# Performance work log

Measured on AMD Instinct MI355X. Metric: run time of the kernel, lower is better.

Reference implementation:

```python
import jax, jax.numpy as jnp
import numpy as np

N_NODES = 50000
N_EDGES = 800000
D = 128


def setup_inputs() -> dict:
    key = jax.random.key(0)
    k1, k2, k3, k4, k5 = jax.random.split(key, 5)
    feature = jax.random.normal(k1, (N_NODES, D), dtype=jnp.float32)
    src = jax.random.randint(k2, (N_EDGES,), 0, N_NODES, dtype=jnp.int64)
    dst = jax.random.randint(k3, (N_EDGES,), 0, N_NODES, dtype=jnp.int64)
    # Linear(in_feats=128, out_feats=128) params
    W = jax.random.normal(k4, (D, D), dtype=jnp.float32) * (1.0 / np.sqrt(D))
    b = jax.random.normal(k5, (D,), dtype=jnp.float32) * 0.01
    return {"feature": feature, "src": src, "dst": dst, "W": W, "b": b}


def reference(feature, src, dst, W, b):
    n = feature.shape[0]
    # copy_src message: each edge carries h[src]; segment-mean over in-edges at dst
    msgs = feature[src]                                      # [E, D] irregular gather
    summed = jax.ops.segment_sum(msgs, dst, num_segments=n)  # [N, D] scatter-add
    cnt = jax.ops.segment_sum(jnp.ones((src.shape[0],), dtype=feature.dtype),
                              dst, num_segments=n)           # in-degree per node
    h = summed / jnp.clip(cnt, 1.0)[:, None]                 # mean (isolated nodes -> 0)
    # NodeApplyModule: ReLU(W h + b)
    return jax.nn.relu(h @ W.T + b)
```

## Files before the change

### kernel.cpp

```cpp
#include <hip/hip_runtime.h>

#define NN 50000
#define NE 800000
#define DD 128
#define NPAD 50176


__global__ __launch_bounds__(256) void k_hist(const int* __restrict__ dst,
                                              int* __restrict__ cnt) {
  int e = blockIdx.x * 256 + threadIdx.x;
  if (e < NE) atomicAdd(&cnt[dst[e]], 1);
}

__global__ __launch_bounds__(256) void k_reduce(const int* __restrict__ cnt,
                                                int* __restrict__ bsum) {
  __shared__ int sh[256];
  int t = threadIdx.x;
  sh[t] = cnt[blockIdx.x * 256 + t];
  __syncthreads();
  for (int o = 128; o > 0; o >>= 1) {
    if (t < o) sh[t] += sh[t + o];
    __syncthreads();
  }
  if (t == 0) bsum[blockIdx.x] = sh[0];
}

__global__ __launch_bounds__(256) void k_scan_bsum(const int* __restrict__ bsum,
                                                   int* __restrict__ bsumx) {
  __shared__ int sh[256];
  int t = threadIdx.x;
  int v = (t < 196) ? bsum[t] : 0;
  sh[t] = v;
  __syncthreads();
  for (int o = 1; o < 256; o <<= 1) {
    int x = (t >= o) ? sh[t - o] : 0;
    __syncthreads();
    sh[t] += x;
    __syncthreads();
  }
  bsumx[t] = sh[t] - v;
}

__global__ __launch_bounds__(256) void k_scan_block(const int* __restrict__ cnt,
                                                    const int* __restrict__ bsumx,
                                                    int* __restrict__ pos) {
  __shared__ int sh[256];
  int t = threadIdx.x;
  int g = blockIdx.x * 256 + t;
  int v = cnt[g];
  sh[t] = v;
  __syncthreads();
  for (int o = 1; o < 256; o <<= 1) {
    int x = (t >= o) ? sh[t - o] : 0;
    __syncthreads();
    sh[t] += x;
    __syncthreads();
  }
  pos[g] = bsumx[blockIdx.x] + sh[t] - v;
}

__global__ __launch_bounds__(256) void k_fill(const int* __restrict__ src,
                                              const int* __restrict__ dst,
                                              int* __restrict__ pos,
                                              int* __restrict__ csr) {
  int e = blockIdx.x * 256 + threadIdx.x;
  if (e < NE) {
    int d = dst[e];
    int p = atomicAdd(&pos[d], 1);
    csr[p] = src[e];
  }
}

__global__ __launch_bounds__(256) void k_gather(const float* __restrict__ feat,
                                                const int* __restrict__ csr,
                                                const int* __restrict__ pos,
                                                const int* __restrict__ cnt,
                                                float* __restrict__ sum) {
  int n = blockIdx.x * 4 + (threadIdx.x >> 6);
  int lane = threadIdx.x & 63;
  int end = pos[n];
  int c = cnt[n];
  float ax = 0.f, ay = 0.f;
  for (int base = end - c; base < end; base += 64) {
    int m = end - base;
    if (m > 64) m = 64;
    int s = (base + lane < end) ? csr[base + lane] : 0;
    int j = 0;
    for (; j + 3 < m; j += 4) {
      int s0 = __shfl(s, j), s1 = __shfl(s, j + 1);
      int s2 = __shfl(s, j + 2), s3 = __shfl(s, j + 3);
      float2 v0 = ((const float2*)(feat + (long long)s0 * DD))[lane];
      float2 v1 = ((const float2*)(feat + (long long)s1 * DD))[lane];
      float2 v2 = ((const float2*)(feat + (long long)s2 * DD))[lane];
      float2 v3 = ((const float2*)(feat + (long long)s3 * DD))[lane];
      ax += (v0.x + v1.x) + (v2.x + v3.x);
      ay += (v0.y + v1.y) + (v2.y + v3.y);
    }
    for (; j < m; ++j) {
      int sj = __shfl(s, j);
      float2 v = ((const float2*)(feat + (long long)sj * DD))[lane];
      ax += v.x;
      ay += v.y;
    }
  }
  float2 o;
  o.x = ax;
  o.y = ay;
  ((float2*)(sum + (long long)n * DD))[lane] = o;
}

__global__ __launch_bounds__(256) void k_scatter(const float* __restrict__ feat,
                                                 const int* __restrict__ src,
                                                 const int* __restrict__ dst,
                                                 float* __restrict__ summed,
                                                 int* __restrict__ cnt) {
  int wave = threadIdx.x >> 6;
  int lane = threadIdx.x & 63;
  int e = blockIdx.x * 4 + wave;
  if (e >= NE) return;
  int s = src[e];
  int d = dst[e];
  float2 v = ((const float2*)(feat + (long long)s * DD))[lane];
  float* op = summed + (long long)d * DD + lane * 2;
  atomicAdd(op, v.x);
  atomicAdd(op + 1, v.y);
  if (lane == 0) atomicAdd(&cnt[d], 1);
}

__global__ __launch_bounds__(256) void k_gemm(float* __restrict__ io,
                                              const int* __restrict__ cnt,
                                              const float* __restrict__ W,
                                              const float* __restrict__ bias) {
  __shared__ float Wt[64][132];
  __shared__ __attribute__((aligned(16))) float hs[64][72];
  int tid = threadIdx.x;
  int row0 = blockIdx.x * 64;
  int tc = tid & 31;
  int tr = tid >> 5;

  float acc[8][4] = {};

  for (int p = 0; p < 2; ++p) {
    if (p) __syncthreads();
    for (int i = 0; i < 8; ++i) {
      int fidx = tid + (i << 8);
      int c = fidx >> 4;
      int kq = fidx & 15;
      float4 w = ((const float4*)W)[c * 32 + p * 16 + kq];
      int kk = kq << 2;
      Wt[kk + 0][c ^ (((kk + 0) & 31) << 2)] = w.x;
      Wt[kk + 1][c ^ (((kk + 1) & 31) << 2)] = w.y;
      Wt[kk + 2][c ^ (((kk + 2) & 31) << 2)] = w.z;
      Wt[kk + 3][c ^ (((kk + 3) & 31) << 2)] = w.w;
    }
    for (int i = 0; i < 4; ++i) {
      int fidx = tid + (i << 8);
      int r = fidx & 63;
      int kq = fidx >> 6;
      int grow = row0 + r;
      float4 v = make_float4(0.f, 0.f, 0.f, 0.f);
      if (grow < NN) {
        v = ((const float4*)io)[(long long)grow * 32 + p * 16 + kq];
        float inv = 1.0f / fmaxf((float)cnt[grow], 1.0f);
        v.x *= inv; v.y *= inv; v.z *= inv; v.w *= inv;
      }
      int kk = kq << 2;
      hs[kk + 0][r] = v.x;
      hs[kk + 1][r] = v.y;
      hs[kk + 2][r] = v.z;
      hs[kk + 3][r] = v.w;
    }
    __syncthreads();

#pragma unroll 4
    for (int kk = 0; kk < 64; ++kk) {
      float4 w4 = *(const float4*)&Wt[kk][(tc << 2) ^ ((kk & 31) << 2)];
      float4 h0 = *(const float4*)&hs[kk][tr << 3];
      float4 h1 = *(const float4*)&hs[kk][(tr << 3) + 4];
      acc[0][0] += h0.x * w4.x; acc[0][1] += h0.x * w4.y; acc[0][2] += h0.x * w4.z; acc[0][3] += h0.x * w4.w;
      acc[1][0] += h0.y * w4.x; acc[1][1] += h0.y * w4.y; acc[1][2] += h0.y * w4.z; acc[1][3] += h0.y * w4.w;
      acc[2][0] += h0.z * w4.x; acc[2][1] += h0.z * w4.y; acc[2][2] += h0.z * w4.z; acc[2][3] += h0.z * w4.w;
      acc[3][0] += h0.w * w4.x; acc[3][1] += h0.w * w4.y; acc[3][2] += h0.w * w4.z; acc[3][3] += h0.w * w4.w;
      acc[4][0] += h1.x * w4.x; acc[4][1] += h1.x * w4.y; acc[4][2] += h1.x * w4.z; acc[4][3] += h1.x * w4.w;
      acc[5][0] += h1.y * w4.x; acc[5][1] += h1.y * w4.y; acc[5][2] += h1.y * w4.z; acc[5][3] += h1.y * w4.w;
      acc[6][0] += h1.z * w4.x; acc[6][1] += h1.z * w4.y; acc[6][2] += h1.z * w4.z; acc[6][3] += h1.z * w4.w;
      acc[7][0] += h1.w * w4.x; acc[7][1] += h1.w * w4.y; acc[7][2] += h1.w * w4.z; acc[7][3] += h1.w * w4.w;
    }
  }

  float4 b4 = ((const float4*)bias)[tc];
#pragma unroll
  for (int r = 0; r < 8; ++r) {
    int row = row0 + (tr << 3) + r;
    if (row < NN) {
      float4 o;
      o.x = fmaxf(acc[r][0] + b4.x, 0.f);
      o.y = fmaxf(acc[r][1] + b4.y, 0.f);
      o.z = fmaxf(acc[r][2] + b4.z, 0.f);
      o.w = fmaxf(acc[r][3] + b4.w, 0.f);
      ((float4*)(io + (long long)row * DD))[tc] = o;
    }
  }
}

extern "C" void kernel_launch(void* const* d_in, const int* in_sizes, int n_in,
                              void* d_out, int out_size, void* d_ws, size_t ws_size,
                              hipStream_t stream) {
  const float* feature = (const float*)d_in[0];
  const int*   src     = (const int*)d_in[1];
  const int*   dst     = (const int*)d_in[2];
  const float* W       = (const float*)d_in[3];
  const float* bias    = (const float*)d_in[4];
  float* out = (float*)d_out;
  int* cnt = (int*)d_ws;

  size_t need = (size_t)(2 * NPAD + 512 + NE) * sizeof(int);
  int nblk_e = (NE + 255) / 256;
  int nblk_gemm = (NN + 63) / 64;

  if (ws_size >= need) {
    int* pos   = cnt + NPAD;
    int* bsum  = pos + NPAD;
    int* bsumx = bsum + 256;
    int* csr   = bsumx + 256;
    hipMemsetAsync(cnt, 0, NPAD * sizeof(int), stream);
    hipLaunchKernelGGL(k_hist, dim3(nblk_e), dim3(256), 0, stream, dst, cnt);
    hipLaunchKernelGGL(k_reduce, dim3(196), dim3(256), 0, stream, cnt, bsum);
    hipLaunchKernelGGL(k_scan_bsum, dim3(1), dim3(256), 0, stream, bsum, bsumx);
    hipLaunchKernelGGL(k_scan_block, dim3(196), dim3(256), 0, stream, cnt, bsumx, pos);
    hipLaunchKernelGGL(k_fill, dim3(nblk_e), dim3(256), 0, stream, src, dst, pos, csr);
    hipLaunchKernelGGL(k_gather, dim3(NN / 4), dim3(256), 0, stream,
                       feature, csr, pos, cnt, out);
    hipLaunchKernelGGL(k_gemm, dim3(nblk_gemm), dim3(256), 0, stream,
                       out, cnt, W, bias);
  } else {
    hipMemsetAsync(out, 0, (size_t)NN * DD * sizeof(float), stream);
    hipMemsetAsync(cnt, 0, NN * sizeof(int), stream);
    hipLaunchKernelGGL(k_scatter, dim3((NE + 3) / 4), dim3(256), 0, stream,
                       feature, src, dst, out, cnt);
    hipLaunchKernelGGL(k_gemm, dim3(nblk_gemm), dim3(256), 0, stream,
                       out, cnt, W, bias);
  }
}
```

Measured before the change: 261.7 us.

## Apply linear transform before aggregation and fuse mean, bias, ReLU into gather

The matmul moves ahead of the aggregation (W·mean(h) = mean(W·h)). A new register-tiled GEMM first computes feature·Wᵀ into a workspace buffer, and the CSR gather then averages those rows while applying bias and ReLU in the same kernel. The three-kernel prefix scan is replaced by a single 1024-thread block scan, and the gather uses float4 loads with two half-waves covering alternate edges. This removes the separate in-place GEMM pass over the aggregated output and two launches, but adds an extra 25.6MB workspace buffer write and needs more workspace.

```diff
diff --git a/kernel.cpp b/kernel.cpp
--- a/kernel.cpp
+++ b/kernel.cpp
@@ -12,51 +12,27 @@
   if (e < NE) atomicAdd(&cnt[dst[e]], 1);
 }
 
-__global__ __launch_bounds__(256) void k_reduce(const int* __restrict__ cnt,
-                                                int* __restrict__ bsum) {
-  __shared__ int sh[256];
+__global__ __launch_bounds__(1024) void k_scan1(const int* __restrict__ cnt,
+                                                int* __restrict__ pos) {
+  __shared__ int sh[1024];
   int t = threadIdx.x;
-  sh[t] = cnt[blockIdx.x * 256 + t];
+  int base = t * 49;
+  int ssum = 0;
+  for (int i = 0; i < 49; ++i) ssum += cnt[base + i];
+  sh[t] = ssum;
   __syncthreads();
-  for (int o = 128; o > 0; o >>= 1) {
-    if (t < o) sh[t] += sh[t + o];
-    __syncthreads();
-  }
-  if (t == 0) bsum[blockIdx.x] = sh[0];
-}
-
-__global__ __launch_bounds__(256) void k_scan_bsum(const int* __restrict__ bsum,
-                                                   int* __restrict__ bsumx) {
-  __shared__ int sh[256];
-  int t = threadIdx.x;
-  int v = (t < 196) ? bsum[t] : 0;
-  sh[t] = v;
-  __syncthreads();
-  for (int o = 1; o < 256; o <<= 1) {
+  for (int o = 1; o < 1024; o <<= 1) {
     int x = (t >= o) ? sh[t - o] : 0;
     __syncthreads();
     sh[t] += x;
     __syncthreads();
   }
-  bsumx[t] = sh[t] - v;
-}
-
-__global__ __launch_bounds__(256) void k_scan_block(const int* __restrict__ cnt,
-                                                    const int* __restrict__ bsumx,
-                                                    int* __restrict__ pos) {
-  __shared__ int sh[256];
-  int t = threadIdx.x;
-  int g = blockIdx.x * 256 + t;
-  int v = cnt[g];
-  sh[t] = v;
-  __syncthreads();
-  for (int o = 1; o < 256; o <<= 1) {
-    int x = (t >= o) ? sh[t - o] : 0;
-    __syncthreads();
-    sh[t] += x;
-    __syncthreads();
-  }
-  pos[g] = bsumx[blockIdx.x] + sh[t] - v;
+  int run = sh[t] - ssum;
+  for (int i = 0; i < 49; ++i) {
+    int v = cnt[base + i];
+    pos[base + i] = run;
+    run += v;
+  }
 }
 
 __global__ __launch_bounds__(256) void k_fill(const int* __restrict__ src,
@@ -71,11 +47,132 @@
   }
 }
 
-__global__ __launch_bounds__(256) void k_gather(const float* __restrict__ feat,
-                                                const int* __restrict__ csr,
-                                                const int* __restrict__ pos,
-                                                const int* __restrict__ cnt,
-                                                float* __restrict__ sum) {
+#define FMA8(R, H)                                          \
+  {                                                         \
+    acc[R][0] += (H)*w0.x; acc[R][1] += (H)*w0.y;           \
+    acc[R][2] += (H)*w0.z; acc[R][3] += (H)*w0.w;           \
+    acc[R][4] += (H)*w1.x; acc[R][5] += (H)*w1.y;           \
+    acc[R][6] += (H)*w1.z; acc[R][7] += (H)*w1.w;           \
+  }
+
+__global__ __launch_bounds__(256) void k_gemmT(const float* __restrict__ feat,
+                                               const float* __restrict__ W,
+                                               float* __restrict__ g) {
+  __shared__ float fs[32][260];
+  __shared__ float ws[32][132];
+  int tid = threadIdx.x;
+  int row0 = blockIdx.x * 256;
+  int tc = tid & 15;
+  int tr = tid >> 4;
+  float acc[16][8] = {};
+
+  for (int kc = 0; kc < 4; ++kc) {
+    if (kc) __syncthreads();
+    for (int i = 0; i < 8; ++i) {
+      int fidx = tid + (i << 8);
+      int r = fidx >> 3;
+      int q = fidx & 7;
+      int grow = row0 + r;
+      float4 v = make_float4(0.f, 0.f, 0.f, 0.f);
+      if (grow < NN) v = ((const float4*)feat)[grow * 32 + kc * 8 + q];
+      int k = q << 2;
+      fs[k + 0][r] = v.x;
+      fs[k + 1][r] = v.y;
+      fs[k + 2][r] = v.z;
+      fs[k + 3][r] = v.w;
+    }
+    for (int i = 0; i < 4; ++i) {
+      int fidx = tid + (i << 8);
+      int c = fidx >> 3;
+      int q = fidx & 7;
+      float4 v = ((const float4*)W)[c * 32 + kc * 8 + q];
+      int k = q << 2;
+      ws[k + 0][c] = v.x;
+      ws[k + 1][c] = v.y;
+      ws[k + 2][c] = v.z;
+      ws[k + 3][c] = v.w;
+    }
+    __syncthreads();
+
+#pragma unroll 8
+    for (int k = 0; k < 32; ++k) {
+      float4 w0 = *(const float4*)&ws[k][tc * 8];
+      float4 w1 = *(const float4*)&ws[k][tc * 8 + 4];
+      float4 h0 = *(const float4*)&fs[k][tr * 16];
+      float4 h1 = *(const float4*)&fs[k][tr * 16 + 4];
+      float4 h2 = *(const float4*)&fs[k][tr * 16 + 8];
+      float4 h3 = *(const float4*)&fs[k][tr * 16 + 12];
+      FMA8(0, h0.x) FMA8(1, h0.y) FMA8(2, h0.z) FMA8(3, h0.w)
+      FMA8(4, h1.x) FMA8(5, h1.y) FMA8(6, h1.z) FMA8(7, h1.w)
+      FMA8(8, h2.x) FMA8(9, h2.y) FMA8(10, h2.z) FMA8(11, h2.w)
+      FMA8(12, h3.x) FMA8(13, h3.y) FMA8(14, h3.z) FMA8(15, h3.w)
+    }
+  }
+
+#pragma unroll
+  for (int r = 0; r < 16; ++r) {
+    int grow = row0 + tr * 16 + r;
+    if (grow < NN) {
+      float4 o0, o1;
+      o0.x = acc[r][0]; o0.y = acc[r][1]; o0.z = acc[r][2]; o0.w = acc[r][3];
+      o1.x = acc[r][4]; o1.y = acc[r][5]; o1.z = acc[r][6]; o1.w = acc[r][7];
+      float4* gp = (float4*)(g + (long long)grow * DD) + tc * 2;
+      gp[0] = o0;
+      gp[1] = o1;
+    }
+  }
+}
+
+__global__ __launch_bounds__(256) void k_gmean(const float* __restrict__ g,
+                                               const int* __restrict__ csr,
+                                               const int* __restrict__ pos,
+                                               const int* __restrict__ cnt,
+                                               const float* __restrict__ bias,
+                                               float* __restrict__ out) {
+  int n = blockIdx.x * 4 + (threadIdx.x >> 6);
+  int lane = threadIdx.x & 63;
+  int half = lane >> 5;
+  int l32 = lane & 31;
+  int end = pos[n];
+  int c = cnt[n];
+  float4 a = make_float4(0.f, 0.f, 0.f, 0.f);
+  for (int base = end - c; base < end; base += 64) {
+    int m = end - base;
+    if (m > 64) m = 64;
+    int s = (base + lane < end) ? csr[base + lane] : 0;
+    for (int j = 0; j < m; j += 8) {
+#pragma unroll
+      for (int u = 0; u < 4; ++u) {
+        int j2 = j + 2 * u + half;
+        int sj = __shfl(s, j2);
+        if (j2 < m) {
+          float4 v = ((const float4*)(g + (long long)sj * DD))[l32];
+          a.x += v.x; a.y += v.y; a.z += v.z; a.w += v.w;
+        }
+      }
+    }
+  }
+  a.x += __shfl_xor(a.x, 32);
+  a.y += __shfl_xor(a.y, 32);
+  a.z += __shfl_xor(a.z, 32);
+  a.w += __shfl_xor(a.w, 32);
+  if (half == 0) {
+    float inv = 1.0f / fmaxf((float)c, 1.0f);
+    float4 b4 = ((const float4*)bias)[l32];
+    float4 o;
+    o.x = fmaxf(a.x * inv + b4.x, 0.f);
+    o.y = fmaxf(a.y * inv + b4.y, 0.f);
+    o.z = fmaxf(a.z * inv + b4.z, 0.f);
+    o.w = fmaxf(a.w * inv + b4.w, 0.f);
+    ((float4*)(out + (long long)n * DD))[l32] = o;
+  }
+}
+
+__global__ __launch_bounds__(256) void k_gather_sum(const float* __restrict__ feat,
+                                                    const int* __restrict__ csr,
+                                                    const int* __restrict__ pos,
+                                                    const int* __restrict__ cnt,
+                                                    float* __restrict__ sum) {
   int n = blockIdx.x * 4 + (threadIdx.x >> 6);
   int lane = threadIdx.x & 63;
   int end = pos[n];
@@ -109,37 +206,17 @@
   ((float2*)(sum + (long long)n * DD))[lane] = o;
 }
 
-__global__ __launch_bounds__(256) void k_scatter(const float* __restrict__ feat,
-                                                 const int* __restrict__ src,
-                                                 const int* __restrict__ dst,
-                                                 float* __restrict__ summed,
-                                                 int* __restrict__ cnt) {
-  int wave = threadIdx.x >> 6;
-  int lane = threadIdx.x & 63;
-  int e = blockIdx.x * 4 + wave;
-  if (e >= NE) return;
-  int s = src[e];
-  int d = dst[e];
-  float2 v = ((const float2*)(feat + (long long)s * DD))[lane];
-  float* op = summed + (long long)d * DD + lane * 2;
-  atomicAdd(op, v.x);
-  atomicAdd(op + 1, v.y);
-  if (lane == 0) atomicAdd(&cnt[d], 1);
-}
-
-__global__ __launch_bounds__(256) void k_gemm(float* __restrict__ io,
-                                              const int* __restrict__ cnt,
-                                              const float* __restrict__ W,
-                                              const float* __restrict__ bias) {
+__global__ __launch_bounds__(256) void k_gemm_inplace(float* __restrict__ io,
+                                                      const int* __restrict__ cnt,
+                                                      const float* __restrict__ W,
+                                                      const float* __restrict__ bias) {
   __shared__ float Wt[64][132];
   __shared__ __attribute__((aligned(16))) float hs[64][72];
   int tid = threadIdx.x;
   int row0 = blockIdx.x * 64;
   int tc = tid & 31;
   int tr = tid >> 5;
-
   float acc[8][4] = {};
-
   for (int p = 0; p < 2; ++p) {
     if (p) __syncthreads();
     for (int i = 0; i < 8; ++i) {
@@ -171,7 +248,6 @@
       hs[kk + 3][r] = v.w;
     }
     __syncthreads();
-
 #pragma unroll 4
     for (int kk = 0; kk < 64; ++kk) {
       float4 w4 = *(const float4*)&Wt[kk][(tc << 2) ^ ((kk & 31) << 2)];
@@ -187,7 +263,6 @@
       acc[7][0] += h1.w * w4.x; acc[7][1] += h1.w * w4.y; acc[7][2] += h1.w * w4.z; acc[7][3] += h1.w * w4.w;
     }
   }
-
   float4 b4 = ((const float4*)bias)[tc];
 #pragma unroll
   for (int r = 0; r < 8; ++r) {
@@ -212,33 +287,30 @@
   const float* W       = (const float*)d_in[3];
   const float* bias    = (const float*)d_in[4];
   float* out = (float*)d_out;
+
   int* cnt = (int*)d_ws;
-
-  size_t need = (size_t)(2 * NPAD + 512 + NE) * sizeof(int);
+  int* pos = cnt + NPAD;
+  int* csr = pos + NPAD;
+  float* g = (float*)(csr + NE);
+
+  size_t need_csr = (size_t)(2 * NPAD + NE) * sizeof(int);
+  size_t need_g = need_csr + (size_t)NN * DD * sizeof(float);
   int nblk_e = (NE + 255) / 256;
-  int nblk_gemm = (NN + 63) / 64;
-
-  if (ws_size >= need) {
-    int* pos   = cnt + NPAD;
-    int* bsum  = pos + NPAD;
-    int* bsumx = bsum + 256;
-    int* csr   = bsumx + 256;
-    hipMemsetAsync(cnt, 0, NPAD * sizeof(int), stream);
-    hipLaunchKernelGGL(k_hist, dim3(nblk_e), dim3(256), 0, stream, dst, cnt);
-    hipLaunchKernelGGL(k_reduce, dim3(196), dim3(256), 0, stream, cnt, bsum);
-    hipLaunchKernelGGL(k_scan_bsum, dim3(1), dim3(256), 0, stream, bsum, bsumx);
-    hipLaunchKernelGGL(k_scan_block, dim3(196), dim3(256), 0, stream, cnt, bsumx, pos);
-    hipLaunchKernelGGL(k_fill, dim3(nblk_e), dim3(256), 0, stream, src, dst, pos, csr);
-    hipLaunchKernelGGL(k_gather, dim3(NN / 4), dim3(256), 0, stream,
+
+  hipMemsetAsync(cnt, 0, NPAD * sizeof(int), stream);
+  hipLaunchKernelGGL(k_hist, dim3(nblk_e), dim3(256), 0, stream, dst, cnt);
+  hipLaunchKernelGGL(k_scan1, dim3(1), dim3(1024), 0, stream, cnt, pos);
+  hipLaunchKernelGGL(k_fill, dim3(nblk_e), dim3(256), 0, stream, src, dst, pos, csr);
+
+  if (ws_size >= need_g) {
+    hipLaunchKernelGGL(k_gemmT, dim3((NN + 255) / 256), dim3(256), 0, stream,
+                       feature, W, g);
+    hipLaunchKernelGGL(k_gmean, dim3(NN / 4), dim3(256), 0, stream,
+                       g, csr, pos, cnt, bias, out);
+  } else {
+    hipLaunchKernelGGL(k_gather_sum, dim3(NN / 4), dim3(256), 0, stream,
                        feature, csr, pos, cnt, out);
-    hipLaunchKernelGGL(k_gemm, dim3(nblk_gemm), dim3(256), 0, stream,
-                       out, cnt, W, bias);
-  } else {
-    hipMemsetAsync(out, 0, (size_t)NN * DD * sizeof(float), stream);
-    hipMemsetAsync(cnt, 0, NN * sizeof(int), stream);
-    hipLaunchKernelGGL(k_scatter, dim3((NE + 3) / 4), dim3(256), 0, stream,
-                       feature, src, dst, out, cnt);
-    hipLaunchKernelGGL(k_gemm, dim3(nblk_gemm), dim3(256), 0, stream,
-                       out, cnt, W, bias);
-  }
-}
+    hipLaunchKernelGGL(k_gemm_inplace, dim3((NN + 63) / 64), dim3(256), 0,
+                       stream, out, cnt, W, bias);
+  }
+}
```

Result: slower. 278.9 us (+6.5%).
